# Optimization experiments

Measured on AMD Instinct MI355X. Metric: run time of the kernel, lower is better.

## Reference

```python
import jax, jax.numpy as jnp
import numpy as np
import math

B, S, D, H = 2, 2048, 1024, 16
DK = D // H

def setup_inputs() -> dict:
    key = jax.random.key(0)
    ks = jax.random.split(key, 12)
    s = 1.0 / math.sqrt(D)
    inp = {
        'input_q': jax.random.normal(ks[0], (B, S, D), jnp.float32),
        'input_k': jax.random.normal(ks[1], (B, S, D), jnp.float32),
        'input_v': jax.random.normal(ks[2], (B, S, D), jnp.float32),
        'mask': jax.random.randint(ks[3], (B, 1, S, S), 0, 2, jnp.int32),
        'Wq': jax.random.normal(ks[4], (D, D), jnp.float32) * s,
        'bq': jnp.zeros((D,), jnp.float32),
        'Wk': jax.random.normal(ks[5], (D, D), jnp.float32) * s,
        'bk': jnp.zeros((D,), jnp.float32),
        'Wv': jax.random.normal(ks[6], (D, D), jnp.float32) * s,
        'bv': jnp.zeros((D,), jnp.float32),
        'Wo': jax.random.normal(ks[7], (D, D), jnp.float32) * s,
        'bo': jnp.zeros((D,), jnp.float32),
    }
    return inp

def reference(input_q, input_k, input_v, mask, Wq, bq, Wk, bk, Wv, bv, Wo, bo):
    # Linear projections (torch Linear: x @ W.T + b), split into heads: [B,H,S,DK]
    q = (input_q @ Wq.T + bq).reshape(B, S, H, DK).transpose(0, 2, 1, 3)
    k = (input_k @ Wk.T + bk).reshape(B, S, H, DK).transpose(0, 2, 1, 3)
    v = (input_v @ Wv.T + bv).reshape(B, S, H, DK).transpose(0, 2, 1, 3)
    scores = jnp.einsum('bhqd,bhkd->bhqk', q, k) / math.sqrt(DK)
    scores = jnp.where(mask == 0, jnp.float32(-1e9), scores)
    attn = jax.nn.softmax(scores, axis=-1)
    out = jnp.einsum('bhqk,bhkd->bhqd', attn, v)
    out = out.transpose(0, 2, 1, 3).reshape(B, S, D)
    return out @ Wo.T + bo
```

## Files before the change

kernel.cpp:

```cpp
#include <hip/hip_runtime.h>
#include <math.h>

#define kB 2
#define kS 2048
#define kD 1024
#define kH 16
#define kM (kB * kS)

typedef unsigned short u16;
typedef unsigned int u32;
typedef unsigned long long u64;
typedef short s16x8 __attribute__((ext_vector_type(8)));
typedef float f32x4 __attribute__((ext_vector_type(4)));

__device__ __forceinline__ u16 f2bf(float f) {
    u32 u = __float_as_uint(f);
    u += 0x7FFFu + ((u >> 16) & 1u);
    return (u16)(u >> 16);
}

__device__ __forceinline__ u32 pack_bf2(float f0, float f1) {
    const u32 r0 = __float_as_uint(f0) + 0x8000u;
    const u32 r1 = __float_as_uint(f1) + 0x8000u;
    return __builtin_amdgcn_perm(r1, r0, 0x07060302u);
}

typedef __attribute__((address_space(1))) void as1_void;
typedef __attribute__((address_space(3))) void as3_void;
__device__ __forceinline__ void async_copy16(const void* g, void* l) {
    __builtin_amdgcn_global_load_lds((as1_void*)(unsigned long long)g,
                                     (as3_void*)(unsigned)(unsigned long long)l,
                                     16, 0, 0);
}

__global__ __launch_bounds__(256) void prep(
        const float* __restrict__ xq, const float* __restrict__ xk, const float* __restrict__ xv,
        const float* __restrict__ Wq, const float* __restrict__ Wk,
        const float* __restrict__ Wv, const float* __restrict__ Wo,
        const int* __restrict__ msk,
        u16* __restrict__ xqb, u16* __restrict__ xkb, u16* __restrict__ xvb,
        u16* __restrict__ wqb, u16* __restrict__ wkb, u16* __restrict__ wvb,
        u16* __restrict__ wob, u64* __restrict__ prepM) {
    const int bid = blockIdx.x;
    const int tid = threadIdx.x;
    if (bid < 16384) {
        const float* in;
        u16* out;
        int i;
        if (bid < 12288) {
            const int z = bid >> 12;
            in = z == 0 ? xq : (z == 1 ? xk : xv);
            out = z == 0 ? xqb : (z == 1 ? xkb : xvb);
            i = (bid & 4095) * 256 + tid;
        } else {
            const int z = (bid - 12288) >> 10;
            in = z == 0 ? Wq : (z == 1 ? Wk : (z == 2 ? Wv : Wo));
            out = z == 0 ? wqb : (z == 1 ? wkb : (z == 2 ? wvb : wob));
            i = ((bid - 12288) & 1023) * 256 + tid;
        }
        const float4 v = ((const float4*)in)[i];
        ushort4 o;
        o.x = f2bf(v.x); o.y = f2bf(v.y); o.z = f2bf(v.z); o.w = f2bf(v.w);
        ((ushort4*)out)[i] = o;
    } else {
        const int wid = (bid - 16384) * 4 + (tid >> 6);
        const int lane = tid & 63;
        const int kt = wid & 31, qb = (wid >> 5) & 127, b = wid >> 12;
        const int q = qb * 16 + (lane & 15);
        const int kbase = kt * 64 + ((lane >> 4) << 2);
        const int* mrow = msk + ((size_t)b * kS + q) * kS;
        u64 keep = 0;
#pragma unroll
        for (int e = 0; e < 16; ++e) {
            const int k = kbase + (e >> 2) * 16 + (e & 3);
            const u64 bl = __ballot(mrow[k] != 0);
            if (lane == e) keep = bl;
        }
        if (lane < 16)
            prepM[(((size_t)b * 128 + qb) * 32 + kt) * 16 + lane] = keep;
    }
}

template <int MODE>
__device__ __forceinline__ void gemm_bt_body(const u16* __restrict__ A,
                                             const u16* __restrict__ W,
                                             const float* __restrict__ bias,
                                             void* __restrict__ Cp) {
    __shared__ u16 As[128 * 32];
    __shared__ u16 Bs[128 * 32];
    const int tid = threadIdx.x;
    const int wave = tid >> 6, lane = tid & 63;
    const int l15 = lane & 15, quad = lane >> 4;
    const int wr = wave >> 1, wc = wave & 1;
    const int m0 = (MODE == 3 ? blockIdx.x : blockIdx.y) * 128;
    const int n0 = (MODE == 3 ? blockIdx.y : blockIdx.x) * 128;

    const int srow = lane >> 2;
    const int schk = (lane & 3) ^ (srow & 3);
    const u16* gA0 = A + (size_t)(m0 + 32 * wave + srow) * kD + schk * 8;
    const u16* gA1 = gA0 + 16 * kD;
    const u16* gB0 = W + (size_t)(n0 + 32 * wave + srow) * kD + schk * 8;
    const u16* gB1 = gB0 + 16 * kD;
    u16* lA0 = As + (32 * wave) * 32;
    u16* lA1 = lA0 + 16 * 32;
    u16* lB0 = Bs + (32 * wave) * 32;
    u16* lB1 = lB0 + 16 * 32;

    const int rdoff = (quad ^ (l15 & 3)) * 8;

    f32x4 acc[4][4];
#pragma unroll
    for (int i = 0; i < 4; ++i)
#pragma unroll
        for (int j = 0; j < 4; ++j) acc[i][j] = (f32x4)0.f;

    for (int kt = 0; kt < kD; kt += 32) {
        __syncthreads();
        async_copy16(gA0 + kt, lA0);
        async_copy16(gA1 + kt, lA1);
        async_copy16(gB0 + kt, lB0);
        async_copy16(gB1 + kt, lB1);
        __syncthreads();

        s16x8 af[4], bf[4];
#pragma unroll
        for (int fm = 0; fm < 4; ++fm)
            af[fm] = *(const s16x8*)(As + (wr * 64 + fm * 16 + l15) * 32 + rdoff);
#pragma unroll
        for (int fn = 0; fn < 4; ++fn)
            bf[fn] = *(const s16x8*)(Bs + (wc * 64 + fn * 16 + l15) * 32 + rdoff);
#pragma unroll
        for (int fm = 0; fm < 4; ++fm)
#pragma unroll
            for (int fn = 0; fn < 4; ++fn)
                acc[fm][fn] = __builtin_amdgcn_mfma_f32_16x16x32_bf16(
                    af[fm], bf[fn], acc[fm][fn], 0, 0, 0);
    }

    if constexpr (MODE == 3) {
#pragma unroll
        for (int fn = 0; fn < 4; ++fn) {
            const int sglob = n0 + wc * 64 + fn * 16 + l15;
            const int bb = sglob >> 11, ss = sglob & (kS - 1);
#pragma unroll
            for (int fm = 0; fm < 4; ++fm) {
                const int dglob = m0 + wr * 64 + fm * 16 + quad * 4;
                const float4 b4 = *(const float4*)(bias + dglob);
                const float bb4[4] = {b4.x, b4.y, b4.z, b4.w};
                const int hh = dglob >> 6, dd = dglob & 63;
                u16* base = (u16*)Cp + ((size_t)(bb * kH + hh) * 64 + dd) * kS + ss;
#pragma unroll
                for (int r = 0; r < 4; ++r)
                    base[(size_t)r * kS] = f2bf(acc[fm][fn][r] + bb4[r]);
            }
        }
    } else {
#pragma unroll
        for (int fn = 0; fn < 4; ++fn) {
            const int col = n0 + wc * 64 + fn * 16 + l15;
            const float bv = bias[col];
#pragma unroll
            for (int fm = 0; fm < 4; ++fm) {
                const int row = m0 + wr * 64 + fm * 16 + quad * 4;
#pragma unroll
                for (int r = 0; r < 4; ++r) {
                    const float v = acc[fm][fn][r] + bv;
                    if constexpr (MODE == 0)
                        ((u16*)Cp)[(size_t)(row + r) * kD + col] = f2bf(v);
                    else
                        ((float*)Cp)[(size_t)(row + r) * kD + col] = v;
                }
            }
        }
    }
}

__global__ __launch_bounds__(256) void qkv_gemm(
        const u16* __restrict__ xq, const u16* __restrict__ xk, const u16* __restrict__ xv,
        const u16* __restrict__ wq, const u16* __restrict__ wk, const u16* __restrict__ wv,
        const float* __restrict__ bq, const float* __restrict__ bk, const float* __restrict__ bv,
        u16* __restrict__ q, u16* __restrict__ k, u16* __restrict__ vt) {
    const int z = blockIdx.z;
    if (z == 0)      gemm_bt_body<0>(xq, wq, bq, q);
    else if (z == 1) gemm_bt_body<0>(xk, wk, bk, k);
    else             gemm_bt_body<3>(wv, xv, bv, vt);
}

__global__ __launch_bounds__(256) void o_gemm(const u16* __restrict__ A,
                                              const u16* __restrict__ W,
                                              const float* __restrict__ bias,
                                              float* __restrict__ C) {
    gemm_bt_body<2>(A, W, bias, C);
}

#define kC 0.180336880f

__global__ __launch_bounds__(256) void attn_mfma(const u16* __restrict__ Qb,
                                                 const u16* __restrict__ Kb,
                                                 const u16* __restrict__ Vt,
                                                 const u64* __restrict__ prepM,
                                                 u16* __restrict__ Ob) {
    __shared__ u16 Qs[64 * 64];
    __shared__ u16 Ks[64 * 64];
    __shared__ u16 Vs[64 * 64];
    __shared__ u16 Ps[64 * 64];

    const int tid = threadIdx.x;
    const int wave = tid >> 6, lane = tid & 63;
    const int l15 = lane & 15, quad = lane >> 4, l7 = lane & 7;
    const int q0 = blockIdx.x * 64;
    const int b = blockIdx.y >> 4, h = blockIdx.y & 15;

    const int srow = lane >> 3;
    const int schk = l7 ^ srow;

    {
        const u16* g0 = Qb + ((size_t)(b * kS + q0 + 16 * wave + srow)) * kD + h * 64 + schk * 8;
        async_copy16(g0, Qs + (16 * wave) * 64);
        async_copy16(g0 + 8 * kD, Qs + (16 * wave + 8) * 64);
    }
    const u16* gK0 = Kb + ((size_t)(b * kS + 16 * wave + srow)) * kD + h * 64 + schk * 8;
    const u16* gV0 = Vt + ((size_t)((b * kH + h) * 64 + 16 * wave + srow)) * kS + schk * 8;

    const int wave_u = __builtin_amdgcn_readfirstlane(wave);
    const u64* mbase = prepM + (((size_t)b * 128 + blockIdx.x * 4 + wave_u) * 32) * 16;

    f32x4 oacc[4];
#pragma unroll
    for (int i = 0; i < 4; ++i) oacc[i] = (f32x4)0.f;
    float l_r = 0.f;

    __syncthreads();
    s16x8 bq[2];
    bq[0] = *(const s16x8*)(Qs + (16 * wave + l15) * 64 + ((0 + quad) ^ l7) * 8);
    bq[1] = *(const s16x8*)(Qs + (16 * wave + l15) * 64 + ((4 + quad) ^ l7) * 8);
    u16* psrow = Ps + (16 * wave + l15) * 64;

    for (int kt = 0; kt < kS; kt += 64) {
        __syncthreads();
        async_copy16(gK0 + (size_t)kt * kD, Ks + (16 * wave) * 64);
        async_copy16(gK0 + (size_t)(kt + 8) * kD, Ks + (16 * wave + 8) * 64);
        async_copy16(gV0 + kt, Vs + (16 * wave) * 64);
        async_copy16(gV0 + 8 * kS + kt, Vs + (16 * wave + 8) * 64);
        __syncthreads();

        f32x4 s[4];
#pragma unroll
        for (int fn = 0; fn < 4; ++fn) s[fn] = (f32x4)0.f;
#pragma unroll
        for (int kc = 0; kc < 2; ++kc)
#pragma unroll
            for (int fn = 0; fn < 4; ++fn) {
                const s16x8 ak = *(const s16x8*)(Ks + (fn * 16 + l15) * 64 + ((kc * 4 + quad) ^ l7) * 8);
                s[fn] = __builtin_amdgcn_mfma_f32_16x16x32_bf16(ak, bq[kc], s[fn], 0, 0, 0);
            }

        const u64* mt = mbase + (kt >> 6) * 16;
        float ps = 0.f;
#pragma unroll
        for (int fn = 0; fn < 4; ++fn)
#pragma unroll
            for (int r = 0; r < 4; ++r) {
                const u64 mm = mt[fn * 4 + r];
                const float p = exp2f(fmaf(s[fn][r], kC, -8.0f));
                float pm;
                asm("v_cndmask_b32 %0, 0, %1, %2" : "=v"(pm) : "v"(p), "s"(mm));
                s[fn][r] = pm;
                ps += pm;
            }
        ps += __shfl_xor(ps, 16);
        ps += __shfl_xor(ps, 32);
        l_r += ps;

#pragma unroll
        for (int fn = 0; fn < 4; ++fn) {
            uint2 o;
            o.x = pack_bf2(s[fn][0], s[fn][1]);
            o.y = pack_bf2(s[fn][2], s[fn][3]);
            const int chunk = fn * 2 + (quad >> 1);
            *(uint2*)(psrow + ((chunk ^ l7) * 8) + (quad & 1) * 4) = o;
        }

#pragma unroll
        for (int kc = 0; kc < 2; ++kc) {
            const s16x8 bp = *(const s16x8*)(psrow + ((kc * 4 + quad) ^ l7) * 8);
#pragma unroll
            for (int fd = 0; fd < 4; ++fd) {
                const s16x8 av = *(const s16x8*)(Vs + (fd * 16 + l15) * 64 + ((kc * 4 + quad) ^ l7) * 8);
                oacc[fd] = __builtin_amdgcn_mfma_f32_16x16x32_bf16(av, bp, oacc[fd], 0, 0, 0);
            }
        }
    }

    const float inv = 1.f / l_r;
    const size_t orow = (size_t)(b * kS + q0 + 16 * wave + l15);
#pragma unroll
    for (int fd = 0; fd < 4; ++fd) {
        uint2 o;
        o.x = pack_bf2(oacc[fd][0] * inv, oacc[fd][1] * inv);
        o.y = pack_bf2(oacc[fd][2] * inv, oacc[fd][3] * inv);
        *(uint2*)(Ob + orow * kD + h * 64 + fd * 16 + quad * 4) = o;
    }
}

extern "C" void kernel_launch(void* const* d_in, const int* in_sizes, int n_in,
                              void* d_out, int out_size, void* d_ws, size_t ws_size,
                              hipStream_t stream) {
    const float* xq = (const float*)d_in[0];
    const float* xk = (const float*)d_in[1];
    const float* xv = (const float*)d_in[2];
    const int*  msk = (const int*)d_in[3];
    const float* Wq = (const float*)d_in[4];
    const float* bq = (const float*)d_in[5];
    const float* Wk = (const float*)d_in[6];
    const float* bk = (const float*)d_in[7];
    const float* Wv = (const float*)d_in[8];
    const float* bv = (const float*)d_in[9];
    const float* Wo = (const float*)d_in[10];
    const float* bo = (const float*)d_in[11];
    float* out = (float*)d_out;

    const size_t NX = (size_t)kM * kD;
    const size_t NW = (size_t)kD * kD;

    u64* prepM = (u64*)d_ws;
    u16* p = (u16*)((char*)d_ws + (1 << 20));
    u16* xqb = p; p += NX;
    u16* xkb = p; p += NX;
    u16* xvb = p; p += NX;
    u16* wqb = p; p += NW;
    u16* wkb = p; p += NW;
    u16* wvb = p; p += NW;
    u16* wob = p; p += NW;
    u16* qb  = p; p += NX;
    u16* kb  = p; p += NX;
    u16* vtb = p; p += NX;
    u16* ab  = xqb;

    prep<<<18432, 256, 0, stream>>>(xq, xk, xv, Wq, Wk, Wv, Wo, msk,
                                    xqb, xkb, xvb, wqb, wkb, wvb, wob, prepM);

    dim3 gq(kD / 128, kM / 128, 3);
    qkv_gemm<<<gq, 256, 0, stream>>>(xqb, xkb, xvb, wqb, wkb, wvb, bq, bk, bv, qb, kb, vtb);

    dim3 ga(kS / 64, kB * kH);
    attn_mfma<<<ga, 256, 0, stream>>>(qb, kb, vtb, prepM, ab);

    dim3 go(kD / 128, kM / 128);
    o_gemm<<<go, 256, 0, stream>>>(ab, wob, bo, out);
}
```

Baseline: 291.1 us.

## Double query rows per attention block, use bf16 mask tiles and MFMA row sums

The attention block now handles 128 query rows, with two 16-row groups per wave, so each K/V tile loaded into LDS is reused twice. The mask is expanded in prep to a dense 16-bit 0/0xFFFF array, streamed into LDS per tile and applied with a bitwise AND on the packed bf16 probabilities. This replaces the ballot-packed bitmask and per-element cndmask. The row-sum shuffles are replaced by an MFMA against a ones vector. In exchange, mask traffic grows (8 MB of bf16 mask read per head pass, 16x re-read across heads), the grid halves, and LDS use rises.

Result: slower. 302.2 us (+3.8%).

```diff
diff --git a/kernel.cpp b/kernel.cpp
--- a/kernel.cpp
+++ b/kernel.cpp
@@ -12,6 +12,7 @@
 typedef unsigned long long u64;
 typedef short s16x8 __attribute__((ext_vector_type(8)));
 typedef float f32x4 __attribute__((ext_vector_type(4)));
+typedef u16 u16x8 __attribute__((ext_vector_type(8)));
 
 __device__ __forceinline__ u16 f2bf(float f) {
     u32 u = __float_as_uint(f);
@@ -40,7 +41,7 @@
         const int* __restrict__ msk,
         u16* __restrict__ xqb, u16* __restrict__ xkb, u16* __restrict__ xvb,
         u16* __restrict__ wqb, u16* __restrict__ wkb, u16* __restrict__ wvb,
-        u16* __restrict__ wob, u64* __restrict__ prepM) {
+        u16* __restrict__ wob, u16* __restrict__ Msx) {
     const int bid = blockIdx.x;
     const int tid = threadIdx.x;
     if (bid < 16384) {
@@ -63,21 +64,18 @@
         o.x = f2bf(v.x); o.y = f2bf(v.y); o.z = f2bf(v.z); o.w = f2bf(v.w);
         ((ushort4*)out)[i] = o;
     } else {
-        const int wid = (bid - 16384) * 4 + (tid >> 6);
-        const int lane = tid & 63;
-        const int kt = wid & 31, qb = (wid >> 5) & 127, b = wid >> 12;
-        const int q = qb * 16 + (lane & 15);
-        const int kbase = kt * 64 + ((lane >> 4) << 2);
-        const int* mrow = msk + ((size_t)b * kS + q) * kS;
-        u64 keep = 0;
-#pragma unroll
-        for (int e = 0; e < 16; ++e) {
-            const int k = kbase + (e >> 2) * 16 + (e & 3);
-            const u64 bl = __ballot(mrow[k] != 0);
-            if (lane == e) keep = bl;
-        }
-        if (lane < 16)
-            prepM[(((size_t)b * 128 + qb) * 32 + kt) * 16 + lane] = keep;
+        const int mid = (bid - 16384) * 256 + tid;
+        const int c = mid & 255;
+        const int row = mid >> 8;
+        const int4* src = (const int4*)(msk + (size_t)row * kS + c * 8);
+        const int4 v0 = src[0];
+        const int4 v1 = src[1];
+        u16x8 o;
+        o[0] = v0.x ? 0xFFFFu : 0; o[1] = v0.y ? 0xFFFFu : 0;
+        o[2] = v0.z ? 0xFFFFu : 0; o[3] = v0.w ? 0xFFFFu : 0;
+        o[4] = v1.x ? 0xFFFFu : 0; o[5] = v1.y ? 0xFFFFu : 0;
+        o[6] = v1.z ? 0xFFFFu : 0; o[7] = v1.w ? 0xFFFFu : 0;
+        *(u16x8*)(Msx + (size_t)row * kS + c * 8) = o;
     }
 }
 
@@ -198,108 +196,129 @@
 __global__ __launch_bounds__(256) void attn_mfma(const u16* __restrict__ Qb,
                                                  const u16* __restrict__ Kb,
                                                  const u16* __restrict__ Vt,
-                                                 const u64* __restrict__ prepM,
+                                                 const u16* __restrict__ Msx,
                                                  u16* __restrict__ Ob) {
-    __shared__ u16 Qs[64 * 64];
+    __shared__ u16 QPs[128 * 64];
     __shared__ u16 Ks[64 * 64];
     __shared__ u16 Vs[64 * 64];
-    __shared__ u16 Ps[64 * 64];
+    __shared__ u16 Ms[128 * 64];
 
     const int tid = threadIdx.x;
     const int wave = tid >> 6, lane = tid & 63;
     const int l15 = lane & 15, quad = lane >> 4, l7 = lane & 7;
-    const int q0 = blockIdx.x * 64;
+    const int q0 = blockIdx.x * 128;
     const int b = blockIdx.y >> 4, h = blockIdx.y & 15;
 
     const int srow = lane >> 3;
     const int schk = l7 ^ srow;
 
-    {
-        const u16* g0 = Qb + ((size_t)(b * kS + q0 + 16 * wave + srow)) * kD + h * 64 + schk * 8;
-        async_copy16(g0, Qs + (16 * wave) * 64);
-        async_copy16(g0 + 8 * kD, Qs + (16 * wave + 8) * 64);
-    }
-    const u16* gK0 = Kb + ((size_t)(b * kS + 16 * wave + srow)) * kD + h * 64 + schk * 8;
-    const u16* gV0 = Vt + ((size_t)((b * kH + h) * 64 + 16 * wave + srow)) * kS + schk * 8;
-
-    const int wave_u = __builtin_amdgcn_readfirstlane(wave);
-    const u64* mbase = prepM + (((size_t)b * 128 + blockIdx.x * 4 + wave_u) * 32) * 16;
-
-    f32x4 oacc[4];
-#pragma unroll
-    for (int i = 0; i < 4; ++i) oacc[i] = (f32x4)0.f;
-    float l_r = 0.f;
+    const u16* gQ = Qb + ((size_t)(b * kS + q0 + 32 * wave + srow)) * kD + h * 64 + schk * 8;
+#pragma unroll
+    for (int i = 0; i < 4; ++i)
+        async_copy16(gQ + (size_t)(8 * i) * kD, QPs + (32 * wave + 8 * i) * 64);
+
+    const u16* gK = Kb + ((size_t)(b * kS + 16 * wave + srow)) * kD + h * 64 + schk * 8;
+    const u16* gV = Vt + ((size_t)((b * kH + h) * 64 + 16 * wave + srow)) * kS + schk * 8;
+    const u16* gM = Msx + ((size_t)(b * kS + q0 + 32 * wave + srow)) * kS + schk * 8;
+
+    f32x4 oacc[2][4];
+#pragma unroll
+    for (int g = 0; g < 2; ++g)
+#pragma unroll
+        for (int i = 0; i < 4; ++i) oacc[g][i] = (f32x4)0.f;
+    f32x4 lacc[2];
+    lacc[0] = (f32x4)0.f; lacc[1] = (f32x4)0.f;
+
+    s16x8 ones;
+#pragma unroll
+    for (int j = 0; j < 8; ++j) ones[j] = (short)0x3F80;
 
     __syncthreads();
-    s16x8 bq[2];
-    bq[0] = *(const s16x8*)(Qs + (16 * wave + l15) * 64 + ((0 + quad) ^ l7) * 8);
-    bq[1] = *(const s16x8*)(Qs + (16 * wave + l15) * 64 + ((4 + quad) ^ l7) * 8);
-    u16* psrow = Ps + (16 * wave + l15) * 64;
+    s16x8 qf[2][2];
+#pragma unroll
+    for (int qg = 0; qg < 2; ++qg)
+#pragma unroll
+        for (int kc = 0; kc < 2; ++kc)
+            qf[qg][kc] = *(const s16x8*)(QPs + (32 * wave + qg * 16 + l15) * 64 +
+                                         ((kc * 4 + quad) ^ l7) * 8);
 
     for (int kt = 0; kt < kS; kt += 64) {
         __syncthreads();
-        async_copy16(gK0 + (size_t)kt * kD, Ks + (16 * wave) * 64);
-        async_copy16(gK0 + (size_t)(kt + 8) * kD, Ks + (16 * wave + 8) * 64);
-        async_copy16(gV0 + kt, Vs + (16 * wave) * 64);
-        async_copy16(gV0 + 8 * kS + kt, Vs + (16 * wave + 8) * 64);
+        async_copy16(gK + (size_t)kt * kD, Ks + (16 * wave) * 64);
+        async_copy16(gK + (size_t)(kt + 8) * kD, Ks + (16 * wave + 8) * 64);
+        async_copy16(gV + kt, Vs + (16 * wave) * 64);
+        async_copy16(gV + 8 * kS + kt, Vs + (16 * wave + 8) * 64);
+#pragma unroll
+        for (int i = 0; i < 4; ++i)
+            async_copy16(gM + (size_t)(8 * i) * kS + kt, Ms + (32 * wave + 8 * i) * 64);
         __syncthreads();
 
-        f32x4 s[4];
-#pragma unroll
-        for (int fn = 0; fn < 4; ++fn) s[fn] = (f32x4)0.f;
+        f32x4 s[2][4];
+#pragma unroll
+        for (int qg = 0; qg < 2; ++qg)
+#pragma unroll
+            for (int fn = 0; fn < 4; ++fn) s[qg][fn] = (f32x4)0.f;
 #pragma unroll
         for (int kc = 0; kc < 2; ++kc)
 #pragma unroll
             for (int fn = 0; fn < 4; ++fn) {
-                const s16x8 ak = *(const s16x8*)(Ks + (fn * 16 + l15) * 64 + ((kc * 4 + quad) ^ l7) * 8);
-                s[fn] = __builtin_amdgcn_mfma_f32_16x16x32_bf16(ak, bq[kc], s[fn], 0, 0, 0);
-            }
-
-        const u64* mt = mbase + (kt >> 6) * 16;
-        float ps = 0.f;
-#pragma unroll
-        for (int fn = 0; fn < 4; ++fn)
-#pragma unroll
-            for (int r = 0; r < 4; ++r) {
-                const u64 mm = mt[fn * 4 + r];
-                const float p = exp2f(fmaf(s[fn][r], kC, -8.0f));
-                float pm;
-                asm("v_cndmask_b32 %0, 0, %1, %2" : "=v"(pm) : "v"(p), "s"(mm));
-                s[fn][r] = pm;
-                ps += pm;
-            }
-        ps += __shfl_xor(ps, 16);
-        ps += __shfl_xor(ps, 32);
-        l_r += ps;
-
-#pragma unroll
-        for (int fn = 0; fn < 4; ++fn) {
+                const s16x8 ak = *(const s16x8*)(Ks + (fn * 16 + l15) * 64 +
+                                                 ((kc * 4 + quad) ^ l7) * 8);
+#pragma unroll
+                for (int qg = 0; qg < 2; ++qg)
+                    s[qg][fn] = __builtin_amdgcn_mfma_f32_16x16x32_bf16(
+                        ak, qf[qg][kc], s[qg][fn], 0, 0, 0);
+            }
+
+#pragma unroll
+        for (int qg = 0; qg < 2; ++qg) {
+            const int base = (32 * wave + qg * 16 + l15) * 64;
+#pragma unroll
+            for (int fn = 0; fn < 4; ++fn) {
+                const float p0 = exp2f(fmaf(s[qg][fn][0], kC, -8.0f));
+                const float p1 = exp2f(fmaf(s[qg][fn][1], kC, -8.0f));
+                const float p2 = exp2f(fmaf(s[qg][fn][2], kC, -8.0f));
+                const float p3 = exp2f(fmaf(s[qg][fn][3], kC, -8.0f));
+                const int off = base + ((fn * 2 + (quad >> 1)) ^ l7) * 8 + (quad & 1) * 4;
+                const uint2 m2 = *(const uint2*)(Ms + off);
+                uint2 o;
+                o.x = pack_bf2(p0, p1) & m2.x;
+                o.y = pack_bf2(p2, p3) & m2.y;
+                *(uint2*)(QPs + off) = o;
+            }
+        }
+
+#pragma unroll
+        for (int kc = 0; kc < 2; ++kc) {
+            s16x8 av[4];
+#pragma unroll
+            for (int fd = 0; fd < 4; ++fd)
+                av[fd] = *(const s16x8*)(Vs + (fd * 16 + l15) * 64 +
+                                         ((kc * 4 + quad) ^ l7) * 8);
+#pragma unroll
+            for (int qg = 0; qg < 2; ++qg) {
+                const s16x8 bp = *(const s16x8*)(QPs + (32 * wave + qg * 16 + l15) * 64 +
+                                                 ((kc * 4 + quad) ^ l7) * 8);
+                lacc[qg] = __builtin_amdgcn_mfma_f32_16x16x32_bf16(ones, bp, lacc[qg], 0, 0, 0);
+#pragma unroll
+                for (int fd = 0; fd < 4; ++fd)
+                    oacc[qg][fd] = __builtin_amdgcn_mfma_f32_16x16x32_bf16(
+                        av[fd], bp, oacc[qg][fd], 0, 0, 0);
+            }
+        }
+    }
+
+#pragma unroll
+    for (int qg = 0; qg < 2; ++qg) {
+        const float inv = 1.f / lacc[qg][0];
+        const size_t orow = (size_t)(b * kS + q0 + 32 * wave + qg * 16 + l15);
+#pragma unroll
+        for (int fd = 0; fd < 4; ++fd) {
             uint2 o;
-            o.x = pack_bf2(s[fn][0], s[fn][1]);
-            o.y = pack_bf2(s[fn][2], s[fn][3]);
-            const int chunk = fn * 2 + (quad >> 1);
-            *(uint2*)(psrow + ((chunk ^ l7) * 8) + (quad & 1) * 4) = o;
-        }
-
-#pragma unroll
-        for (int kc = 0; kc < 2; ++kc) {
-            const s16x8 bp = *(const s16x8*)(psrow + ((kc * 4 + quad) ^ l7) * 8);
-#pragma unroll
-            for (int fd = 0; fd < 4; ++fd) {
-                const s16x8 av = *(const s16x8*)(Vs + (fd * 16 + l15) * 64 + ((kc * 4 + quad) ^ l7) * 8);
-                oacc[fd] = __builtin_amdgcn_mfma_f32_16x16x32_bf16(av, bp, oacc[fd], 0, 0, 0);
-            }
-        }
-    }
-
-    const float inv = 1.f / l_r;
-    const size_t orow = (size_t)(b * kS + q0 + 16 * wave + l15);
-#pragma unroll
-    for (int fd = 0; fd < 4; ++fd) {
-        uint2 o;
-        o.x = pack_bf2(oacc[fd][0] * inv, oacc[fd][1] * inv);
-        o.y = pack_bf2(oacc[fd][2] * inv, oacc[fd][3] * inv);
-        *(uint2*)(Ob + orow * kD + h * 64 + fd * 16 + quad * 4) = o;
+            o.x = pack_bf2(oacc[qg][fd][0] * inv, oacc[qg][fd][1] * inv);
+            o.y = pack_bf2(oacc[qg][fd][2] * inv, oacc[qg][fd][3] * inv);
+            *(uint2*)(Ob + orow * kD + h * 64 + fd * 16 + quad * 4) = o;
+        }
     }
 }
 
@@ -322,9 +341,10 @@
 
     const size_t NX = (size_t)kM * kD;
     const size_t NW = (size_t)kD * kD;
-
-    u64* prepM = (u64*)d_ws;
-    u16* p = (u16*)((char*)d_ws + (1 << 20));
+    const size_t NM = (size_t)kB * kS * kS;
+
+    u16* p = (u16*)d_ws;
+    u16* Msx = p; p += NM;
     u16* xqb = p; p += NX;
     u16* xkb = p; p += NX;
     u16* xvb = p; p += NX;
@@ -337,14 +357,14 @@
     u16* vtb = p; p += NX;
     u16* ab  = xqb;
 
-    prep<<<18432, 256, 0, stream>>>(xq, xk, xv, Wq, Wk, Wv, Wo, msk,
-                                    xqb, xkb, xvb, wqb, wkb, wvb, wob, prepM);
+    prep<<<20480, 256, 0, stream>>>(xq, xk, xv, Wq, Wk, Wv, Wo, msk,
+                                    xqb, xkb, xvb, wqb, wkb, wvb, wob, Msx);
 
     dim3 gq(kD / 128, kM / 128, 3);
     qkv_gemm<<<gq, 256, 0, stream>>>(xqb, xkb, xvb, wqb, wkb, wvb, bq, bk, bv, qb, kb, vtb);
 
-    dim3 ga(kS / 64, kB * kH);
-    attn_mfma<<<ga, 256, 0, stream>>>(qb, kb, vtb, prepM, ab);
+    dim3 ga(kS / 128, kB * kH);
+    attn_mfma<<<ga, 256, 0, stream>>>(qb, kb, vtb, Msx, ab);
 
     dim3 go(kD / 128, kM / 128);
     o_gemm<<<go, 256, 0, stream>>>(ab, wob, bo, out);
```

## Deepen GEMM K-tile to 64 with XOR swizzle and shrink O-proj M-tile

Applied to the files above, without the earlier changes.

The shared GEMM body now stages 64-wide K slices per iteration instead of 32, which halves the number of barrier pairs and uses an 8-chunk XOR swizzle for LDS reads. It is also templated on the M tile size. The output projection uses a 64-row M tile, doubling its grid from 256 to 512 blocks so more CUs are occupied. The cost is twice the LDS per block and fewer accumulators per wave in o_gemm, which lowers per-wave MFMA reuse.

After: 280.6 us. 3.6% less time.

```diff
diff --git a/kernel.cpp b/kernel.cpp
--- a/kernel.cpp
+++ b/kernel.cpp
@@ -81,60 +81,61 @@
     }
 }
 
-template <int MODE>
+template <int MODE, int TILEM>
 __device__ __forceinline__ void gemm_bt_body(const u16* __restrict__ A,
                                              const u16* __restrict__ W,
                                              const float* __restrict__ bias,
                                              void* __restrict__ Cp) {
-    __shared__ u16 As[128 * 32];
-    __shared__ u16 Bs[128 * 32];
+    constexpr int FM = TILEM / 32;
+    __shared__ u16 As[TILEM * 64];
+    __shared__ u16 Bs[128 * 64];
     const int tid = threadIdx.x;
     const int wave = tid >> 6, lane = tid & 63;
-    const int l15 = lane & 15, quad = lane >> 4;
+    const int l15 = lane & 15, quad = lane >> 4, l7 = lane & 7;
     const int wr = wave >> 1, wc = wave & 1;
-    const int m0 = (MODE == 3 ? blockIdx.x : blockIdx.y) * 128;
+    const int m0 = (MODE == 3 ? blockIdx.x : blockIdx.y) * TILEM;
     const int n0 = (MODE == 3 ? blockIdx.y : blockIdx.x) * 128;
 
-    const int srow = lane >> 2;
-    const int schk = (lane & 3) ^ (srow & 3);
-    const u16* gA0 = A + (size_t)(m0 + 32 * wave + srow) * kD + schk * 8;
-    const u16* gA1 = gA0 + 16 * kD;
-    const u16* gB0 = W + (size_t)(n0 + 32 * wave + srow) * kD + schk * 8;
-    const u16* gB1 = gB0 + 16 * kD;
-    u16* lA0 = As + (32 * wave) * 32;
-    u16* lA1 = lA0 + 16 * 32;
-    u16* lB0 = Bs + (32 * wave) * 32;
-    u16* lB1 = lB0 + 16 * 32;
-
-    const int rdoff = (quad ^ (l15 & 3)) * 8;
-
-    f32x4 acc[4][4];
-#pragma unroll
-    for (int i = 0; i < 4; ++i)
+    const int srow = lane >> 3;
+    const int schk = l7 ^ srow;
+    const u16* gA = A + (size_t)(m0 + (TILEM / 4) * wave + srow) * kD + schk * 8;
+    const u16* gB = W + (size_t)(n0 + 32 * wave + srow) * kD + schk * 8;
+    u16* lA = As + ((TILEM / 4) * wave) * 64;
+    u16* lB = Bs + (32 * wave) * 64;
+
+    f32x4 acc[FM][4];
+#pragma unroll
+    for (int i = 0; i < FM; ++i)
 #pragma unroll
         for (int j = 0; j < 4; ++j) acc[i][j] = (f32x4)0.f;
 
-    for (int kt = 0; kt < kD; kt += 32) {
+    for (int kt = 0; kt < kD; kt += 64) {
         __syncthreads();
-        async_copy16(gA0 + kt, lA0);
-        async_copy16(gA1 + kt, lA1);
-        async_copy16(gB0 + kt, lB0);
-        async_copy16(gB1 + kt, lB1);
+#pragma unroll
+        for (int i = 0; i < TILEM / 32; ++i)
+            async_copy16(gA + (size_t)(8 * i) * kD + kt, lA + (8 * i) * 64);
+#pragma unroll
+        for (int i = 0; i < 4; ++i)
+            async_copy16(gB + (size_t)(8 * i) * kD + kt, lB + (8 * i) * 64);
         __syncthreads();
 
-        s16x8 af[4], bf[4];
-#pragma unroll
-        for (int fm = 0; fm < 4; ++fm)
-            af[fm] = *(const s16x8*)(As + (wr * 64 + fm * 16 + l15) * 32 + rdoff);
-#pragma unroll
-        for (int fn = 0; fn < 4; ++fn)
-            bf[fn] = *(const s16x8*)(Bs + (wc * 64 + fn * 16 + l15) * 32 + rdoff);
-#pragma unroll
-        for (int fm = 0; fm < 4; ++fm)
+#pragma unroll
+        for (int s = 0; s < 2; ++s) {
+            const int rdoff = ((s * 4 + quad) ^ l7) * 8;
+            s16x8 af[FM], bf[4];
+#pragma unroll
+            for (int fm = 0; fm < FM; ++fm)
+                af[fm] = *(const s16x8*)(As + (wr * (TILEM / 2) + fm * 16 + l15) * 64 + rdoff);
 #pragma unroll
             for (int fn = 0; fn < 4; ++fn)
-                acc[fm][fn] = __builtin_amdgcn_mfma_f32_16x16x32_bf16(
-                    af[fm], bf[fn], acc[fm][fn], 0, 0, 0);
+                bf[fn] = *(const s16x8*)(Bs + (wc * 64 + fn * 16 + l15) * 64 + rdoff);
+#pragma unroll
+            for (int fm = 0; fm < FM; ++fm)
+#pragma unroll
+                for (int fn = 0; fn < 4; ++fn)
+                    acc[fm][fn] = __builtin_amdgcn_mfma_f32_16x16x32_bf16(
+                        af[fm], bf[fn], acc[fm][fn], 0, 0, 0);
+        }
     }
 
     if constexpr (MODE == 3) {
@@ -143,8 +144,8 @@
             const int sglob = n0 + wc * 64 + fn * 16 + l15;
             const int bb = sglob >> 11, ss = sglob & (kS - 1);
 #pragma unroll
-            for (int fm = 0; fm < 4; ++fm) {
-                const int dglob = m0 + wr * 64 + fm * 16 + quad * 4;
+            for (int fm = 0; fm < FM; ++fm) {
+                const int dglob = m0 + wr * (TILEM / 2) + fm * 16 + quad * 4;
                 const float4 b4 = *(const float4*)(bias + dglob);
                 const float bb4[4] = {b4.x, b4.y, b4.z, b4.w};
                 const int hh = dglob >> 6, dd = dglob & 63;
@@ -160,8 +161,8 @@
             const int col = n0 + wc * 64 + fn * 16 + l15;
             const float bv = bias[col];
 #pragma unroll
-            for (int fm = 0; fm < 4; ++fm) {
-                const int row = m0 + wr * 64 + fm * 16 + quad * 4;
+            for (int fm = 0; fm < FM; ++fm) {
+                const int row = m0 + wr * (TILEM / 2) + fm * 16 + quad * 4;
 #pragma unroll
                 for (int r = 0; r < 4; ++r) {
                     const float v = acc[fm][fn][r] + bv;
@@ -181,16 +182,16 @@
         const float* __restrict__ bq, const float* __restrict__ bk, const float* __restrict__ bv,
         u16* __restrict__ q, u16* __restrict__ k, u16* __restrict__ vt) {
     const int z = blockIdx.z;
-    if (z == 0)      gemm_bt_body<0>(xq, wq, bq, q);
-    else if (z == 1) gemm_bt_body<0>(xk, wk, bk, k);
-    else             gemm_bt_body<3>(wv, xv, bv, vt);
+    if (z == 0)      gemm_bt_body<0, 128>(xq, wq, bq, q);
+    else if (z == 1) gemm_bt_body<0, 128>(xk, wk, bk, k);
+    else             gemm_bt_body<3, 128>(wv, xv, bv, vt);
 }
 
 __global__ __launch_bounds__(256) void o_gemm(const u16* __restrict__ A,
                                               const u16* __restrict__ W,
                                               const float* __restrict__ bias,
                                               float* __restrict__ C) {
-    gemm_bt_body<2>(A, W, bias, C);
+    gemm_bt_body<2, 64>(A, W, bias, C);
 }
 
 #define kC 0.180336880f
@@ -346,6 +347,6 @@
     dim3 ga(kS / 64, kB * kH);
     attn_mfma<<<ga, 256, 0, stream>>>(qb, kb, vtb, prepM, ab);
 
-    dim3 go(kD / 128, kM / 128);
+    dim3 go(kD / 128, kM / 64);
     o_gemm<<<go, 256, 0, stream>>>(ab, wob, bo, out);
 }
```
